# Optimization experiments

Hardware: AMD Instinct MI355X
Metric: run time of the kernel (lower is better)

## Reference

```python
import jax, jax.numpy as jnp
import numpy as np

B_SZ = 8
G = 2048
D_MODEL = 512
D_STATE = 128
D_CONV = 4
EXPAND = 2
HEADDIM = 64
D_INNER = EXPAND * D_MODEL          # 1024
NHEADS = D_INNER // HEADDIM         # 16
CONV_DIM = D_INNER + 2 * D_STATE    # 1280
D_IN_PROJ = 2 * D_INNER + 2 * D_STATE + NHEADS  # 2320
ID_DIM = 128
CHR_DIM = 64
N_CHR = 25
F_LOCUS = 32
PATH_DIM = 128
GENE_FEAT = ID_DIM + PATH_DIM + 2 * CHR_DIM  # 384
N_PERT = 10000
P_DIM = 128


def silu(x):
    return x * jax.nn.sigmoid(x)


def causal_dw_conv(x, w, b):
    # x: (B,L,C), w: (C,K), b: (C,)  causal depthwise conv (left pad K-1)
    K = w.shape[1]
    L = x.shape[1]
    xp = jnp.pad(x, ((0, 0), (K - 1, 0), (0, 0)))
    out = b[None, None, :]
    for k in range(K):
        out = out + xp[:, k:k + L, :] * w[:, k][None, None, :]
    return out


def mamba2(u, in_w, conv_w, conv_b, dt_bias, A_log, Dp, norm_w, out_w):
    # u: (B,L,d_model) -> (B,L,d_model); mamba_ssm Mamba2 defaults, ngroups=1
    Bb, L, _ = u.shape
    zxbcdt = u @ in_w.T                                   # (B,L,D_IN_PROJ)
    z = zxbcdt[..., :D_INNER]
    xBC = zxbcdt[..., D_INNER:D_INNER + CONV_DIM]
    dt = zxbcdt[..., D_INNER + CONV_DIM:]                 # (B,L,H)
    xBC = silu(causal_dw_conv(xBC, conv_w, conv_b))
    x = xBC[..., :D_INNER].reshape(Bb, L, NHEADS, HEADDIM)
    Bm = xBC[..., D_INNER:D_INNER + D_STATE]              # (B,L,N)
    Cm = xBC[..., D_INNER + D_STATE:]                     # (B,L,N)
    dt = jax.nn.softplus(dt + dt_bias)                    # (B,L,H)
    dA = jnp.exp(dt * (-jnp.exp(A_log)))                  # (B,L,H)

    def step(h, inp):
        dA_t, dt_t, B_t, C_t, x_t = inp
        h = dA_t[:, :, None, None] * h + jnp.einsum('bh,bn,bhp->bhpn', dt_t, B_t, x_t)
        y = jnp.einsum('bhpn,bn->bhp', h, C_t)
        return h, y

    h0 = jnp.zeros((Bb, NHEADS, HEADDIM, D_STATE), u.dtype)
    xs = (dA.transpose(1, 0, 2), dt.transpose(1, 0, 2),
          Bm.transpose(1, 0, 2), Cm.transpose(1, 0, 2), x.transpose(1, 0, 2, 3))
    _, ys = jax.lax.scan(step, h0, xs)                    # ys: (L,B,H,P)
    y = ys.transpose(1, 0, 2, 3) + Dp[None, None, :, None] * x
    y = y.reshape(Bb, L, D_INNER)
    # gated RMSNorm (norm_before_gate=False): norm(y * silu(z))
    y = y * silu(z)
    y = y * jax.lax.rsqrt(jnp.mean(y * y, axis=-1, keepdims=True) + 1e-5) * norm_w
    return y @ out_w.T


def setup_inputs() -> dict:
    key = jax.random.key(0)
    ks = iter(jax.random.split(key, 48))

    def nrm(shape, scale):
        return jax.random.normal(next(ks), shape, jnp.float32) * scale

    inp = {}
    inp['perturbation_idx'] = jax.random.randint(next(ks), (B_SZ,), 0, N_PERT)
    inp['chr_idx'] = jax.random.randint(next(ks), (G,), 0, N_CHR)
    inp['locus_fourier'] = nrm((G, 2 * F_LOCUS), 1.0)
    inp['pathway_features'] = nrm((G, PATH_DIM), 1.0)
    inp['pert_emb'] = nrm((N_PERT, P_DIM), 0.02)
    inp['gene_id_emb'] = nrm((G, ID_DIM), 0.02)
    inp['chr_emb'] = nrm((N_CHR, CHR_DIM), 0.02)
    inp['locus_w'] = nrm((CHR_DIM, 2 * F_LOCUS), (2 * F_LOCUS) ** -0.5)
    inp['locus_b'] = jnp.zeros((CHR_DIM,), jnp.float32)
    inp['cond_w'] = nrm((GENE_FEAT, P_DIM), P_DIM ** -0.5)
    inp['cond_b'] = jnp.zeros((GENE_FEAT,), jnp.float32)
    inp['in_w'] = nrm((D_MODEL, GENE_FEAT), GENE_FEAT ** -0.5)
    inp['in_b'] = jnp.zeros((D_MODEL,), jnp.float32)
    inp['head_w'] = nrm((1, D_MODEL), D_MODEL ** -0.5)
    inp['head_b'] = jnp.zeros((1,), jnp.float32)
    for p in ('f_', 'b_'):
        inp[p + 'in_w'] = nrm((D_IN_PROJ, D_MODEL), D_MODEL ** -0.5)
        inp[p + 'conv_w'] = nrm((CONV_DIM, D_CONV), D_CONV ** -0.5)
        inp[p + 'conv_b'] = jnp.zeros((CONV_DIM,), jnp.float32)
        inp[p + 'dt_bias'] = nrm((NHEADS,), 0.5)
        inp[p + 'A_log'] = jnp.log(jax.random.uniform(next(ks), (NHEADS,), jnp.float32, 1.0, 16.0))
        inp[p + 'D'] = jnp.ones((NHEADS,), jnp.float32)
        inp[p + 'norm_w'] = jnp.ones((D_INNER,), jnp.float32)
        inp[p + 'out_w'] = nrm((D_MODEL, D_INNER), D_INNER ** -0.5)
    return inp


def reference(perturbation_idx, chr_idx, locus_fourier, pathway_features,
              pert_emb, gene_id_emb, chr_emb, locus_w, locus_b,
              cond_w, cond_b, in_w, in_b, head_w, head_b,
              f_in_w, f_conv_w, f_conv_b, f_dt_bias, f_A_log, f_D, f_norm_w, f_out_w,
              b_in_w, b_conv_w, b_conv_b, b_dt_bias, b_A_log, b_D, b_norm_w, b_out_w):
    B = perturbation_idx.shape[0]
    cond = pert_emb[perturbation_idx] @ cond_w.T + cond_b          # (B, GENE_FEAT)
    e_chr = chr_emb[chr_idx]                                        # (G, CHR_DIM)
    e_locus = jax.nn.gelu(locus_fourier @ locus_w.T + locus_b, approximate=False)
    gene_feat = jnp.concatenate([gene_id_emb, pathway_features, e_chr, e_locus], axis=1)  # (G, GENE_FEAT)
    seq = jnp.concatenate([cond[:, None, :],
                           jnp.broadcast_to(gene_feat[None], (B,) + gene_feat.shape)], axis=1)
    seq = seq @ in_w.T + in_b                                       # (B, G+1, d_model)
    h_fwd = mamba2(seq, f_in_w, f_conv_w, f_conv_b, f_dt_bias, f_A_log, f_D, f_norm_w, f_out_w)
    h_bwd = jnp.flip(mamba2(jnp.flip(seq, axis=1), b_in_w, b_conv_w, b_conv_b,
                            b_dt_bias, b_A_log, b_D, b_norm_w, b_out_w), axis=1)
    H = h_fwd + h_bwd
    return H[:, 1:, :] @ head_w.T + head_b                          # (B, G, 1)
```

## Files before the change

kernel.cpp:

```cpp
#include <hip/hip_runtime.h>
#include <hip/hip_bf16.h>
#include <hip/hip_fp16.h>
#include <math.h>

#define DPROJ 2320
#define CONVD 1280

typedef __attribute__((ext_vector_type(8))) short bf16x8;
typedef __attribute__((ext_vector_type(4))) float f32x4;

__device__ __forceinline__ float siluf(float x) { return x / (1.f + __expf(-x)); }
__device__ __forceinline__ float bfu(unsigned short s) { return __uint_as_float(((unsigned)s) << 16); }
__device__ __forceinline__ unsigned short f2bf(float f) {
    unsigned u = __float_as_uint(f);
    unsigned r = (u + 0x7FFFu + ((u >> 16) & 1u)) >> 16;
    return (unsigned short)r;
}
__device__ __forceinline__ unsigned short f2h(float f) {
    __half h = __float2half(f);
    return *(unsigned short*)&h;
}
__device__ __forceinline__ float h2f(unsigned short s) {
    __half h = *(__half*)&s;
    return __half2float(h);
}


__global__ void gg_kernel(const int* __restrict__ chridx, const float* __restrict__ gid,
                          const float* __restrict__ path, const float* __restrict__ chrE,
                          const int* __restrict__ pidx, const float* __restrict__ pertE,
                          float* __restrict__ gf, float* __restrict__ cemb,
                          float* __restrict__ wf2, float* __restrict__ wb2) {
    int blk = blockIdx.x, tid = threadIdx.x;
    if (blk < 3072) {
        int idx = blk * 256 + tid;
        int g = idx / 384, j = idx % 384;
        float v;
        if (j < 128)      v = gid[(size_t)g * 128 + j];
        else if (j < 256) v = path[(size_t)g * 128 + (j - 128)];
        else if (j < 320) v = chrE[(size_t)chridx[g] * 64 + (j - 256)];
        else return;
        gf[idx] = v;
    } else if (blk < 3076) {
        int idx = (blk - 3072) * 256 + tid;
        int b = idx >> 7, k = idx & 127;
        cemb[idx] = pertE[(size_t)pidx[b] * 128 + k];
    } else {
        wf2[tid * 4 + 0] = 0.f; wf2[tid * 4 + 1] = 0.f;
        wf2[tid * 4 + 2] = 0.f; wf2[tid * 4 + 3] = 0.f;
        wb2[tid * 4 + 0] = 0.f; wb2[tid * 4 + 1] = 0.f;
        wb2[tid * 4 + 2] = 0.f; wb2[tid * 4 + 3] = 0.f;
    }
}

__global__ void wfold_kernel(const float* __restrict__ headW,
                             const float* __restrict__ fOutW, const float* __restrict__ fNw,
                             const float* __restrict__ bOutW, const float* __restrict__ bNw,
                             float* __restrict__ wf2, float* __restrict__ wb2) {
    int blk = blockIdx.x;
    int dir = blk >> 6;
    int rem = blk & 63;
    int dseg = rem >> 4, mseg = rem & 15;
    int tid = threadIdx.x;
    int d = dseg * 256 + tid;
    const float* W = dir ? bOutW : fOutW;
    float s = 0.f;
#pragma unroll
    for (int m = mseg * 32; m < mseg * 32 + 32; ++m)
        s += headW[m] * W[(size_t)m * 1024 + d];
    const float* nw = dir ? bNw : fNw;
    atomicAdd(&(dir ? wb2 : wf2)[d], s * nw[d]);
}


__global__ void tobf4_kernel(const float* __restrict__ inW, const float* __restrict__ fInW,
                             const float* __restrict__ bInW, const float* __restrict__ gf,
                             unsigned short* __restrict__ inW2, unsigned short* __restrict__ fInW2,
                             unsigned short* __restrict__ bInW2, unsigned short* __restrict__ gf2) {
    size_t idx = (size_t)blockIdx.x * 256 + threadIdx.x;
    const size_t A = 512UL * 384, B5 = 2432UL * 512;
    if (idx < A) {
        inW2[idx] = f2bf(inW[idx]);
    } else if (idx < A + B5) {
        size_t k = idx - A; int m = k / 512, kk = k % 512;
        fInW2[k] = f2bf(m < 2320 ? fInW[(size_t)m * 512 + kk] : 0.f);
    } else if (idx < A + 2 * B5) {
        size_t k = idx - A - B5; int m = k / 512, kk = k % 512;
        bInW2[k] = f2bf(m < 2320 ? bInW[(size_t)m * 512 + kk] : 0.f);
    } else {
        size_t k = idx - A - 2 * B5;
        gf2[k] = f2bf(gf[k]);
    }
}


__global__ __launch_bounds__(256) void mfma_gemm_kernel(
    const unsigned short* __restrict__ A2, const unsigned short* __restrict__ W2,
    const float* __restrict__ bias, float* __restrict__ C,
    unsigned short* __restrict__ Cbf, unsigned short* __restrict__ sz,
    int N, int K2, int ldc) {
    __shared__ __align__(16) unsigned short Al[128 * 40];
    __shared__ __align__(16) unsigned short Bl[128 * 40];
    const int tid = threadIdx.x;
    const int bm = blockIdx.y * 128, bn = blockIdx.x * 128;
    const int lane = tid & 63, wave = tid >> 6;
    const int wm = (wave >> 1) * 64, wn = (wave & 1) * 64;
    f32x4 acc[4][4];
#pragma unroll
    for (int i = 0; i < 4; ++i)
#pragma unroll
        for (int j = 0; j < 4; ++j) acc[i][j] = (f32x4){0.f, 0.f, 0.f, 0.f};

    for (int k0 = 0; k0 < K2; k0 += 32) {
        __syncthreads();
#pragma unroll
        for (int s = 0; s < 2; ++s) {
            int ch = tid + 256 * s;
            int row = ch >> 2, q = ch & 3;
            uint4 va = *(const uint4*)&A2[(size_t)(bm + row) * K2 + k0 + q * 8];
            *(uint4*)&Al[row * 40 + q * 8] = va;
            uint4 vb = *(const uint4*)&W2[(size_t)(bn + row) * K2 + k0 + q * 8];
            *(uint4*)&Bl[row * 40 + q * 8] = vb;
        }
        __syncthreads();
        bf16x8 af[4], bfr[4];
#pragma unroll
        for (int i = 0; i < 4; ++i)
            af[i] = *(const bf16x8*)&Al[(wm + i * 16 + (lane & 15)) * 40 + (lane >> 4) * 8];
#pragma unroll
        for (int j = 0; j < 4; ++j)
            bfr[j] = *(const bf16x8*)&Bl[(wn + j * 16 + (lane & 15)) * 40 + (lane >> 4) * 8];
#pragma unroll
        for (int i = 0; i < 4; ++i)
#pragma unroll
            for (int j = 0; j < 4; ++j)
                acc[i][j] = __builtin_amdgcn_mfma_f32_16x16x32_bf16(af[i], bfr[j], acc[i][j], 0, 0, 0);
    }
#pragma unroll
    for (int i = 0; i < 4; ++i) {
        int m = bm + wm + i * 16 + (lane >> 4) * 4;
#pragma unroll
        for (int j = 0; j < 4; ++j) {
            int n = bn + wn + j * 16 + (lane & 15);
            if (n < N) {
                float bv = bias ? bias[n] : 0.f;
#pragma unroll
                for (int r = 0; r < 4; ++r) {
                    float v = acc[i][j][r] + bv;
                    if (sz && n < 1024)
                        sz[(size_t)(m + r) * 1024 + n] = f2h(siluf(v));
                    else if (Cbf)
                        Cbf[(size_t)(m + r) * ldc + n] = f2bf(v);
                    else
                        C[(size_t)(m + r) * ldc + n] = v;
                }
            }
        }
    }
}


__global__ __launch_bounds__(256) void gemm_kernel(
    const float* __restrict__ A, const float* __restrict__ W,
    const float* __restrict__ bias, float* __restrict__ C,
    int M, int N, int K, int ldc, int act) {
    __shared__ __align__(16) float As[16][68];
    __shared__ __align__(16) float Ws[16][68];
    const int tid = threadIdx.x;
    const int tx = tid & 15, ty = tid >> 4;
    const int bm = blockIdx.y * 64, bn = blockIdx.x * 64;
    const int lr = tid >> 2;
    const int lk = (tid & 3) * 4;
    float acc[4][4];
#pragma unroll
    for (int i = 0; i < 4; ++i)
#pragma unroll
        for (int j = 0; j < 4; ++j) acc[i][j] = 0.f;

    for (int k0 = 0; k0 < K; k0 += 16) {
        const int am = bm + lr;
        const int wn = bn + lr;
        float4 av = make_float4(0.f, 0.f, 0.f, 0.f), wv = make_float4(0.f, 0.f, 0.f, 0.f);
        if (am < M) av = *(const float4*)&A[(size_t)am * K + k0 + lk];
        if (wn < N) wv = *(const float4*)&W[(size_t)wn * K + k0 + lk];
        __syncthreads();
        As[lk + 0][lr] = av.x; As[lk + 1][lr] = av.y; As[lk + 2][lr] = av.z; As[lk + 3][lr] = av.w;
        Ws[lk + 0][lr] = wv.x; Ws[lk + 1][lr] = wv.y; Ws[lk + 2][lr] = wv.z; Ws[lk + 3][lr] = wv.w;
        __syncthreads();
#pragma unroll
        for (int kk = 0; kk < 16; ++kk) {
            float4 a = *(const float4*)&As[kk][ty * 4];
            float4 w = *(const float4*)&Ws[kk][tx * 4];
            float aa[4] = {a.x, a.y, a.z, a.w}, ww[4] = {w.x, w.y, w.z, w.w};
#pragma unroll
            for (int i = 0; i < 4; ++i)
#pragma unroll
                for (int j = 0; j < 4; ++j) acc[i][j] += aa[i] * ww[j];
        }
    }
#pragma unroll
    for (int i = 0; i < 4; ++i) {
        const int m = bm + ty * 4 + i;
        if (m >= M) continue;
#pragma unroll
        for (int j = 0; j < 4; ++j) {
            const int n = bn + tx * 4 + j;
            if (n >= N) continue;
            float v = acc[i][j] + (bias ? bias[n] : 0.f);
            if (act == 1) v = 0.5f * v * (1.f + erff(v * 0.70710678118654752f));
            C[(size_t)m * ldc + n] = v;
        }
    }
}


__global__ void dt_kernel(const float* __restrict__ zxf, const float* __restrict__ zxb,
                          const float* __restrict__ zxc,
                          const float* __restrict__ fDtB, const float* __restrict__ bDtB,
                          float* __restrict__ dtFsT, float* __restrict__ dtBsT,
                          float* __restrict__ dtFp) {
    int idx = blockIdx.x * 256 + threadIdx.x;
    if (idx < 32768) {
        int r = idx >> 4, hh = idx & 15;
        float raw = zxf[(size_t)r * DPROJ + 2304 + hh] + fDtB[hh];
        dtFsT[hh * 2048 + r] = (raw > 20.f) ? raw : log1pf(expf(raw));
    } else if (idx < 65536) {
        int k = idx - 32768;
        int r = k >> 4, hh = k & 15;
        float raw = zxb[(size_t)(2047 - r) * DPROJ + 2304 + hh] + bDtB[hh];
        dtBsT[hh * 2048 + r] = (raw > 20.f) ? raw : log1pf(expf(raw));
    } else if (idx < 65664) {
        int k = idx - 65536;
        int b = k >> 4, hh = k & 15;
        float raw = zxc[(size_t)b * DPROJ + 2304 + hh] + fDtB[hh];
        dtFp[k] = (raw > 20.f) ? raw : log1pf(expf(raw));
    }
}

__global__ void cum_kernel(const float* __restrict__ dtFsT, const float* __restrict__ dtBsT,
                           const float* __restrict__ fAlog, const float* __restrict__ bAlog,
                           float* __restrict__ cumF, float* __restrict__ cumB) {
    int id = blockIdx.x * 256 + threadIdx.x;
    int dir = id >> 9, k = id & 511, h = k >> 5, c = k & 31;
    const float* dtT = dir ? dtBsT : dtFsT;
    const float* Al = dir ? bAlog : fAlog;
    float* cum = dir ? cumB : cumF;
    float a = -expf(Al[h]);
    float acc = 0.f;
    for (int s4 = 0; s4 < 16; ++s4) {
        float4 v = *(const float4*)&dtT[h * 2048 + c * 64 + s4 * 4];
        float4 o;
        acc += v.x * a; o.x = acc;
        acc += v.y * a; o.y = acc;
        acc += v.z * a; o.z = acc;
        acc += v.w * a; o.w = acc;
        *(float4*)&cum[h * 2048 + c * 64 + s4 * 4] = o;
    }
}


__global__ void convFsh_kernel(const float* __restrict__ zxf, const float* __restrict__ cw,
                               const float* __restrict__ cb,
                               unsigned short* __restrict__ bc16, unsigned short* __restrict__ x16) {
    int idx = blockIdx.x * 256 + threadIdx.x;
    if (idx >= 2045 * 1280) return;
    int t4 = idx / 1280, c = idx % 1280;
    float4 w4 = *(const float4*)&cw[c * 4];
    float acc = cb[c];
    acc += zxf[(size_t)(t4 + 0) * DPROJ + 1024 + c] * w4.x;
    acc += zxf[(size_t)(t4 + 1) * DPROJ + 1024 + c] * w4.y;
    acc += zxf[(size_t)(t4 + 2) * DPROJ + 1024 + c] * w4.z;
    acc += zxf[(size_t)(t4 + 3) * DPROJ + 1024 + c] * w4.w;
    float r = siluf(acc);
    if (c >= 1024) bc16[(size_t)t4 * 256 + (c - 1024)] = f2bf(r);
    else           x16[(size_t)t4 * 1024 + c] = f2bf(r);
}

__global__ void convFpb_kernel(const float* __restrict__ zxf, const float* __restrict__ zxc,
                               const float* __restrict__ cw, const float* __restrict__ cb,
                               float* __restrict__ outp, unsigned short* __restrict__ bc16,
                               unsigned short* __restrict__ x16) {
    int idx = blockIdx.x * 256 + threadIdx.x;
    int b = idx / 5120;
    int r = idx % 5120;
    int t = r / 1280, c = r % 1280;
    float4 w4 = *(const float4*)&cw[c * 4];
    float w[4] = {w4.x, w4.y, w4.z, w4.w};
    float acc = cb[c];
#pragma unroll
    for (int k = 0; k < 4; ++k) {
        int j = t - 3 + k;
        float x = 0.f;
        if (j == 0)      x = zxc[(size_t)b * DPROJ + 1024 + c];
        else if (j >= 1) x = zxf[(size_t)(j - 1) * DPROJ + 1024 + c];
        acc += x * w[k];
    }
    float rr = siluf(acc);
    outp[idx] = rr;
    if (c >= 1024) bc16[(size_t)(b * 4 + t) * 256 + (c - 1024)] = f2bf(rr);
    else           x16[(size_t)(b * 4 + t) * 1024 + c] = f2bf(rr);
}

__global__ void convBsh_kernel(const float* __restrict__ zxb, const float* __restrict__ cw,
                               const float* __restrict__ cb,
                               unsigned short* __restrict__ bc16, unsigned short* __restrict__ x16) {
    int idx = blockIdx.x * 256 + threadIdx.x;
    int s = idx / 1280, c = idx % 1280;
    float4 w4 = *(const float4*)&cw[c * 4];
    float w[4] = {w4.x, w4.y, w4.z, w4.w};
    float acc = cb[c];
#pragma unroll
    for (int k = 0; k < 4; ++k) {
        int j = s - 3 + k;
        if (j >= 0) acc += zxb[(size_t)(2047 - j) * DPROJ + 1024 + c] * w[k];
    }
    float r = siluf(acc);
    if (c >= 1024) bc16[(size_t)s * 256 + (c - 1024)] = f2bf(r);
    else           x16[(size_t)s * 1024 + c] = f2bf(r);
}


__global__ __launch_bounds__(256) void intra_kernel(
    const unsigned short* __restrict__ bcF, const unsigned short* __restrict__ bcFp,
    const unsigned short* __restrict__ bcB,
    const unsigned short* __restrict__ xF16, const unsigned short* __restrict__ xFp16,
    const unsigned short* __restrict__ xB16,
    const float* __restrict__ dtFsT, const float* __restrict__ dtBsT,
    const float* __restrict__ cumF, const float* __restrict__ cumB,
    unsigned short* __restrict__ YiF0, unsigned short* __restrict__ YiFs,
    unsigned short* __restrict__ YiB,
    unsigned short* __restrict__ UF0, unsigned short* __restrict__ UFs,
    unsigned short* __restrict__ UB) {
    __shared__ __align__(16) unsigned char smraw[63232];
    unsigned short* Bt = (unsigned short*)smraw;
    unsigned short* Ct = (unsigned short*)(smraw + 17408);
    unsigned short* Sm = (unsigned short*)(smraw + 17408);
    unsigned short* BT = (unsigned short*)(smraw + 34816);
    unsigned short* XT = (unsigned short*)(smraw + 53248);
    float* scum = (float*)(smraw + 62464);
    float* sdt  = scum + 64;
    float* se   = scum + 128;

    const int iid = blockIdx.x;
    int dir, b = 0, h, c;
    unsigned short *Yout, *Uout;
    if (iid < 128)      { dir = 0; b = iid >> 4; h = iid & 15; c = 0;
                          Yout = YiF0 + (size_t)(b * 16 + h) * 4096; Uout = UF0 + (size_t)(b * 16 + h) * 8192; }
    else if (iid < 624) { int k = iid - 128; dir = 0; c = 1 + (k >> 4); h = k & 15;
                          Yout = YiFs + (size_t)(c * 16 + h) * 4096; Uout = UFs + (size_t)(c * 16 + h) * 8192; }
    else                { int k = iid - 624; dir = 1; c = k >> 4; h = k & 15;
                          Yout = YiB + (size_t)(c * 16 + h) * 4096;  Uout = UB + (size_t)(c * 16 + h) * 8192; }
    const float* dtAT = dir ? dtBsT : dtFsT;
    const float* cumA = dir ? cumB : cumF;

    const int tid = threadIdx.x;
    const int lane = tid & 63, wave = tid >> 6;
    const int quad = lane >> 4, l15 = lane & 15;

    {
        int r = tid >> 2, q = tid & 3;
        const unsigned short *bsrc, *xsrc;
        if (dir == 0) {
            int t = 64 * c + 1 + r;
            if (t < 4) { bsrc = bcFp + (size_t)(b * 4 + t) * 256; xsrc = xFp16 + (size_t)(b * 4 + t) * 1024; }
            else       { bsrc = bcF + (size_t)(t - 4) * 256;      xsrc = xF16 + (size_t)(t - 4) * 1024; }
        } else {
            int s = 64 * c + r;
            bsrc = bcB + (size_t)s * 256;
            xsrc = xB16 + (size_t)s * 1024;
        }
#pragma unroll
        for (int i = 0; i < 4; ++i) {
            int n0 = q * 32 + i * 8;
            uint4 v = *(const uint4*)&bsrc[n0];
            *(uint4*)&Bt[r * 136 + n0] = v;
            const unsigned short* pv = (const unsigned short*)&v;
#pragma unroll
            for (int jj = 0; jj < 8; ++jj) BT[(n0 + jj) * 72 + r] = pv[jj];
        }
#pragma unroll
        for (int i = 0; i < 4; ++i) {
            int n0 = q * 32 + i * 8;
            uint4 v = *(const uint4*)&bsrc[128 + n0];
            *(uint4*)&Ct[r * 136 + n0] = v;
        }
#pragma unroll
        for (int k = 0; k < 2; ++k) {
            uint4 v = *(const uint4*)&xsrc[h * 64 + q * 16 + k * 8];
            const unsigned short* pv = (const unsigned short*)&v;
#pragma unroll
            for (int jj = 0; jj < 8; ++jj) XT[(q * 16 + k * 8 + jj) * 72 + r] = pv[jj];
        }
        if (tid < 64) {
            int j = 64 * c + tid;
            scum[tid] = cumA[h * 2048 + j];
            sdt[tid] = dtAT[h * 2048 + j];
        }
    }
    __syncthreads();
    if (tid < 64) se[tid] = __expf(scum[63] - scum[tid]) * sdt[tid];

    const int tm = (wave >> 1) * 32, sn = (wave & 1) * 32;
    f32x4 acc1[2][2];
#pragma unroll
    for (int i = 0; i < 2; ++i)
#pragma unroll
        for (int j = 0; j < 2; ++j) acc1[i][j] = (f32x4){0.f, 0.f, 0.f, 0.f};
#pragma unroll
    for (int ks = 0; ks < 4; ++ks) {
        bf16x8 af[2], bfr[2];
#pragma unroll
        for (int i = 0; i < 2; ++i)
            af[i] = *(const bf16x8*)&Ct[(tm + i * 16 + l15) * 136 + ks * 32 + quad * 8];
#pragma unroll
        for (int j = 0; j < 2; ++j)
            bfr[j] = *(const bf16x8*)&Bt[(sn + j * 16 + l15) * 136 + ks * 32 + quad * 8];
#pragma unroll
        for (int i = 0; i < 2; ++i)
#pragma unroll
            for (int j = 0; j < 2; ++j)
                acc1[i][j] = __builtin_amdgcn_mfma_f32_16x16x32_bf16(af[i], bfr[j], acc1[i][j], 0, 0, 0);
    }
    __syncthreads();

#pragma unroll
    for (int j = 0; j < 2; ++j) {
        int s = sn + j * 16 + l15;
        float cs = scum[s], ds = sdt[s];
#pragma unroll
        for (int i = 0; i < 2; ++i) {
#pragma unroll
            for (int r = 0; r < 4; ++r) {
                int t = tm + i * 16 + quad * 4 + r;
                float v = (s <= t) ? __expf(scum[t] - cs) * ds * acc1[i][j][r] : 0.f;
                Sm[t * 72 + s] = f2bf(v);
            }
        }
    }
    __syncthreads();

    const int pm = (wave >> 1) * 32, tn = (wave & 1) * 32;
    f32x4 acc2[2][2];
#pragma unroll
    for (int i = 0; i < 2; ++i)
#pragma unroll
        for (int j = 0; j < 2; ++j) acc2[i][j] = (f32x4){0.f, 0.f, 0.f, 0.f};
#pragma unroll
    for (int ks = 0; ks < 2; ++ks) {
        bf16x8 af[2], bfr[2];
#pragma unroll
        for (int i = 0; i < 2; ++i)
            af[i] = *(const bf16x8*)&XT[(pm + i * 16 + l15) * 72 + ks * 32 + quad * 8];
#pragma unroll
        for (int j = 0; j < 2; ++j)
            bfr[j] = *(const bf16x8*)&Sm[(tn + j * 16 + l15) * 72 + ks * 32 + quad * 8];
#pragma unroll
        for (int i = 0; i < 2; ++i)
#pragma unroll
            for (int j = 0; j < 2; ++j)
                acc2[i][j] = __builtin_amdgcn_mfma_f32_16x16x32_bf16(af[i], bfr[j], acc2[i][j], 0, 0, 0);
    }
#pragma unroll
    for (int i = 0; i < 2; ++i)
#pragma unroll
        for (int j = 0; j < 2; ++j) {
            int t = tn + j * 16 + l15;
            int p0 = pm + i * 16 + quad * 4;
            ushort4 o = make_ushort4(f2bf(acc2[i][j][0]), f2bf(acc2[i][j][1]),
                                     f2bf(acc2[i][j][2]), f2bf(acc2[i][j][3]));
            *(ushort4*)&Yout[t * 64 + p0] = o;
        }

    const int nm = wave * 32;
    f32x4 acc3[2][4];
#pragma unroll
    for (int i = 0; i < 2; ++i)
#pragma unroll
        for (int j = 0; j < 4; ++j) acc3[i][j] = (f32x4){0.f, 0.f, 0.f, 0.f};
#pragma unroll
    for (int ks = 0; ks < 2; ++ks) {
        float ev[8];
#pragma unroll
        for (int jj = 0; jj < 8; ++jj) ev[jj] = se[ks * 32 + quad * 8 + jj];
        bf16x8 bfx[4];
#pragma unroll
        for (int j = 0; j < 4; ++j) {
            bf16x8 xs = *(const bf16x8*)&XT[(j * 16 + l15) * 72 + ks * 32 + quad * 8];
#pragma unroll
            for (int jj = 0; jj < 8; ++jj)
                bfx[j][jj] = (short)f2bf(bfu((unsigned short)xs[jj]) * ev[jj]);
        }
        bf16x8 af[2];
#pragma unroll
        for (int i = 0; i < 2; ++i)
            af[i] = *(const bf16x8*)&BT[(nm + i * 16 + l15) * 72 + ks * 32 + quad * 8];
#pragma unroll
        for (int i = 0; i < 2; ++i)
#pragma unroll
            for (int j = 0; j < 4; ++j)
                acc3[i][j] = __builtin_amdgcn_mfma_f32_16x16x32_bf16(af[i], bfx[j], acc3[i][j], 0, 0, 0);
    }
#pragma unroll
    for (int i = 0; i < 2; ++i)
#pragma unroll
        for (int j = 0; j < 4; ++j) {
            int p = j * 16 + l15;
            int n0 = nm + i * 16 + quad * 4;
            ushort4 o = make_ushort4(f2bf(acc3[i][j][0]), f2bf(acc3[i][j][1]),
                                     f2bf(acc3[i][j][2]), f2bf(acc3[i][j][3]));
            *(ushort4*)&Uout[p * 128 + n0] = o;
        }
}


__global__ void cbm_kernel(const float* __restrict__ convFp, const unsigned short* __restrict__ bcF,
                           const float* __restrict__ dtFp, const float* __restrict__ cumF,
                           const unsigned short* __restrict__ UF0,
                           float* __restrict__ cb0, unsigned short* __restrict__ Mb) {
    int blk = blockIdx.x, tid = threadIdx.x;
    if (blk < 32) {
        int idx = blk * 256 + tid;
        int b = idx >> 10, r = idx & 1023, h = r >> 6, tl = r & 63;
        int t = tl + 1;
        const float* b0 = convFp + (size_t)(b * 4) * CONVD;
        float s = 0.f;
        if (t < 4) {
            const float* crow = convFp + (size_t)(b * 4 + t) * CONVD;
            for (int n = 0; n < 128; ++n) s += crow[1152 + n] * b0[1024 + n];
        } else {
            const unsigned short* cr = bcF + (size_t)(t - 4) * 256 + 128;
            for (int n = 0; n < 128; ++n) s += bfu(cr[n]) * b0[1024 + n];
        }
        cb0[(b * 16 + h) * 64 + tl] = s * dtFp[b * 16 + h];
    } else {
        int bh = blk - 32;
        int b = bh >> 4, h = bh & 15;
        float D0 = __expf(cumF[h * 2048 + 63]);
        float dt0 = dtFp[b * 16 + h];
        const float* row0 = convFp + (size_t)(b * 4) * CONVD;
        const unsigned short* u = UF0 + (size_t)(b * 16 + h) * 8192;
        unsigned short* m = Mb + (size_t)(b * 16 + h) * 8192;
        for (int e4 = tid; e4 < 2048; e4 += 256) {
            int e = e4 * 4, p = e >> 7, n0 = e & 127;
            float s = D0 * dt0 * row0[h * 64 + p];
            float4 B4 = *(const float4*)&row0[1024 + n0];
            ushort4 uv = *(const ushort4*)&u[e];
            ushort4 o = make_ushort4(f2bf(s * B4.x + bfu(uv.x)), f2bf(s * B4.y + bfu(uv.y)),
                                     f2bf(s * B4.z + bfu(uv.z)), f2bf(s * B4.w + bfu(uv.w)));
            *(ushort4*)&m[e] = o;
        }
    }
}


__global__ void tpsi_kernel(const unsigned short* __restrict__ UFs, const unsigned short* __restrict__ UB,
                            const float* __restrict__ cumF, const float* __restrict__ cumB,
                            unsigned short* __restrict__ Tst, float* __restrict__ psiF) {
    int blk = blockIdx.x;
    int dir = blk >> 7, h = (blk >> 3) & 15, q8 = blk & 7;
    int tid = threadIdx.x;
    const unsigned short* U = dir ? UB : UFs;
    const float* cum = dir ? cumB : cumF;
    unsigned short* T = Tst + (size_t)(dir * 16 + h) * 32 * 8192;
    if (dir == 0 && q8 == 0 && tid == 0) {
        float ps = 1.f;
        for (int c = 1; c < 32; ++c) {
            psiF[h * 32 + c] = ps;
            ps *= __expf(cumF[h * 2048 + c * 64 + 63]);
        }
    }
    const size_t e = (size_t)q8 * 1024 + 4 * tid;
    float4 st = make_float4(0.f, 0.f, 0.f, 0.f);
    const int c0 = dir ? 0 : 1;
    ushort4 u = *(const ushort4*)&U[((size_t)c0 * 16 + h) * 8192 + e];
    for (int c = c0; c < 32; ++c) {
        ushort4 un = make_ushort4(0, 0, 0, 0);
        if (c + 1 < 32) un = *(const ushort4*)&U[((size_t)(c + 1) * 16 + h) * 8192 + e];
        float Dc = __expf(cum[h * 2048 + c * 64 + 63]);
        ushort4 o = make_ushort4(f2bf(st.x), f2bf(st.y), f2bf(st.z), f2bf(st.w));
        *(ushort4*)&T[(size_t)c * 8192 + e] = o;
        st.x = Dc * st.x + bfu(u.x);
        st.y = Dc * st.y + bfu(u.y);
        st.z = Dc * st.z + bfu(u.z);
        st.w = Dc * st.w + bfu(u.w);
        u = un;
    }
}


__global__ __launch_bounds__(256) void yt_kernel(
    const unsigned short* __restrict__ bcF, const unsigned short* __restrict__ bcB,
    const unsigned short* __restrict__ Tst,
    unsigned short* __restrict__ YtF, unsigned short* __restrict__ YtB) {
    const int iid = blockIdx.x;
    int dir, h, c;
    if (iid < 496) { dir = 0; c = 1 + (iid >> 4); h = iid & 15; }
    else           { int k = iid - 496; dir = 1; c = k >> 4; h = k & 15; }
    const unsigned short* Cbase = (dir == 0)
        ? bcF + ((size_t)(64 * c - 3)) * 256 + 128
        : bcB + ((size_t)(64 * c)) * 256 + 128;
    const unsigned short* Tp = Tst + ((size_t)(dir * 16 + h) * 32 + c) * 8192;
    unsigned short* Yt = (dir == 0 ? YtF : YtB) + (size_t)(c * 16 + h) * 4096;
    const int tid = threadIdx.x;
    const int lane = tid & 63, wave = tid >> 6;
    const int quad = lane >> 4, l15 = lane & 15;
    const int pm = (wave >> 1) * 32, tb = (wave & 1) * 32;
    f32x4 acc[2][2];
#pragma unroll
    for (int i = 0; i < 2; ++i)
#pragma unroll
        for (int j = 0; j < 2; ++j) acc[i][j] = (f32x4){0.f, 0.f, 0.f, 0.f};
#pragma unroll
    for (int ks = 0; ks < 4; ++ks) {
        bf16x8 af[2], bfr[2];
#pragma unroll
        for (int i = 0; i < 2; ++i)
            af[i] = *(const bf16x8*)&Tp[(size_t)(pm + i * 16 + l15) * 128 + ks * 32 + quad * 8];
#pragma unroll
        for (int j = 0; j < 2; ++j)
            bfr[j] = *(const bf16x8*)&Cbase[(size_t)(tb + j * 16 + l15) * 256 + ks * 32 + quad * 8];
#pragma unroll
        for (int i = 0; i < 2; ++i)
#pragma unroll
            for (int j = 0; j < 2; ++j)
                acc[i][j] = __builtin_amdgcn_mfma_f32_16x16x32_bf16(af[i], bfr[j], acc[i][j], 0, 0, 0);
    }
#pragma unroll
    for (int i = 0; i < 2; ++i)
#pragma unroll
        for (int j = 0; j < 2; ++j) {
            int t = tb + j * 16 + l15;
            int p0 = pm + i * 16 + quad * 4;
            ushort4 o = make_ushort4(f2bf(acc[i][j][0]), f2bf(acc[i][j][1]),
                                     f2bf(acc[i][j][2]), f2bf(acc[i][j][3]));
            *(ushort4*)&Yt[t * 64 + p0] = o;
        }
}


__global__ __launch_bounds__(256) void gate_kernel(
    const unsigned short* __restrict__ bcF,
    const unsigned short* __restrict__ Mb, const float* __restrict__ psiF,
    const unsigned short* __restrict__ YtF, const unsigned short* __restrict__ YtB,
    const unsigned short* __restrict__ xF16, const unsigned short* __restrict__ xFp16,
    const unsigned short* __restrict__ xB16,
    const unsigned short* __restrict__ szF, const unsigned short* __restrict__ szB,
    const float* __restrict__ convFp,
    const float* __restrict__ cumF, const float* __restrict__ cumB,
    const unsigned short* __restrict__ YiF0, const unsigned short* __restrict__ YiFs,
    const unsigned short* __restrict__ YiB,
    const float* __restrict__ cb0,
    const float* __restrict__ fD, const float* __restrict__ bD,
    const float* __restrict__ wf2, const float* __restrict__ wb2,
    float* __restrict__ aF, float* __restrict__ aB) {
    __shared__ __align__(16) float Ysm[64 * 68];

    const int iid = blockIdx.x;
    int dir, b = 0, h, cg;
    if (iid < 1024) { dir = 0; b = iid >> 7; int r = iid & 127; h = r >> 3; cg = r & 7; }
    else            { int k = iid - 1024; dir = 1; h = k >> 3; cg = k & 7; }
    const int tid = threadIdx.x, tx = tid & 15, ty = tid >> 4;
    const int lane = tid & 63, wave = tid >> 6;
    const int quad = lane >> 4, l15 = lane & 15;

    const float Dh = (dir ? bD : fD)[h];
    const float* wvp = dir ? wb2 : wf2;
    float4 wreg = *(const float4*)&wvp[h * 64 + tx * 4];
    const float* cumA = dir ? cumB : cumF;

    const int pm = (wave >> 1) * 32, tb = (wave & 1) * 32;
    bf16x8 mfr[4][2];
    if (dir == 0) {
        const unsigned short* Mp = Mb + (size_t)(b * 16 + h) * 8192;
#pragma unroll
        for (int ks = 0; ks < 4; ++ks)
#pragma unroll
            for (int i = 0; i < 2; ++i)
                mfr[ks][i] = *(const bf16x8*)&Mp[(size_t)(pm + i * 16 + l15) * 128 + ks * 32 + quad * 8];
    }

    for (int cc = 0; cc < 4; ++cc) {
        const int c = cg * 4 + cc;
        const bool fwdG = (dir == 0 && c > 0);
        if (fwdG) {
            if (cc > 0) __syncthreads();
            const unsigned short* Cbase = bcF + ((size_t)(64 * c - 3)) * 256 + 128;
            f32x4 acc[2][2];
#pragma unroll
            for (int i = 0; i < 2; ++i)
#pragma unroll
                for (int j = 0; j < 2; ++j) acc[i][j] = (f32x4){0.f, 0.f, 0.f, 0.f};
#pragma unroll
            for (int ks = 0; ks < 4; ++ks) {
                bf16x8 bfr[2];
#pragma unroll
                for (int j = 0; j < 2; ++j)
                    bfr[j] = *(const bf16x8*)&Cbase[(size_t)(tb + j * 16 + l15) * 256 + ks * 32 + quad * 8];
#pragma unroll
                for (int i = 0; i < 2; ++i)
#pragma unroll
                    for (int j = 0; j < 2; ++j)
                        acc[i][j] = __builtin_amdgcn_mfma_f32_16x16x32_bf16(mfr[ks][i], bfr[j], acc[i][j], 0, 0, 0);
            }
#pragma unroll
            for (int i = 0; i < 2; ++i)
#pragma unroll
                for (int j = 0; j < 2; ++j)
                    *(f32x4*)&Ysm[(tb + j * 16 + l15) * 68 + pm + i * 16 + quad * 4] = acc[i][j];
            __syncthreads();
        }

        const float psi = fwdG ? psiF[h * 32 + c] : 0.f;
        const unsigned short* Ytp = fwdG ? (YtF + (size_t)(c * 16 + h) * 4096)
                                         : (dir ? (YtB + (size_t)(c * 16 + h) * 4096) : nullptr);
        float4 x0v = make_float4(0.f, 0.f, 0.f, 0.f);
        float cbv[4] = {0.f, 0.f, 0.f, 0.f};
        if (dir == 0 && c == 0) {
            x0v = *(const float4*)&convFp[(size_t)(b * 4) * CONVD + h * 64 + tx * 4];
#pragma unroll
            for (int i = 0; i < 4; ++i) cbv[i] = cb0[(b * 16 + h) * 64 + (ty + 16 * i)];
        }

        float rawet[4];
        ushort4 yi4a[4], x4a[4], z4a[4], yt4a[4];
        float4 cm4a[4];
#pragma unroll
        for (int i = 0; i < 4; ++i) {
            int tl = ty + 16 * i;
            int j = 64 * c + tl;
            rawet[i] = cumA[h * 2048 + j];
            const unsigned short *Yi, *xp, *zp;
            if (dir == 0) {
                Yi = (c == 0) ? YiF0 + (size_t)(b * 16 + h) * 4096 : YiFs + (size_t)(c * 16 + h) * 4096;
                if (c == 0) {
                    int t = j + 1;
                    xp = (t < 4) ? xFp16 + (size_t)(b * 4 + t) * 1024 : xF16 + (size_t)(t - 4) * 1024;
                } else {
                    xp = xF16 + (size_t)(64 * c + tl - 3) * 1024;
                }
                zp = szF + (size_t)j * 1024;
            } else {
                Yi = YiB + (size_t)(c * 16 + h) * 4096;
                xp = xB16 + (size_t)j * 1024;
                zp = szB + (size_t)(2047 - j) * 1024;
            }
            yi4a[i] = *(const ushort4*)&Yi[tl * 64 + tx * 4];
            x4a[i] = *(const ushort4*)&xp[h * 64 + tx * 4];
            z4a[i] = *(const ushort4*)&zp[h * 64 + tx * 4];
            yt4a[i] = Ytp ? *(const ushort4*)&Ytp[tl * 64 + tx * 4] : make_ushort4(0, 0, 0, 0);
            cm4a[i] = fwdG ? *(const float4*)&Ysm[tl * 68 + tx * 4] : make_float4(0.f, 0.f, 0.f, 0.f);
        }

#pragma unroll
        for (int i = 0; i < 4; ++i) {
            int j = 64 * c + ty + 16 * i;
            float et = __expf(rawet[i]);
            float yv[4] = {bfu(yi4a[i].x), bfu(yi4a[i].y), bfu(yi4a[i].z), bfu(yi4a[i].w)};
            float xa[4] = {bfu(x4a[i].x), bfu(x4a[i].y), bfu(x4a[i].z), bfu(x4a[i].w)};
            float sza[4] = {h2f(z4a[i].x), h2f(z4a[i].y), h2f(z4a[i].z), h2f(z4a[i].w)};
            float ya[4] = {bfu(yt4a[i].x) + psi * cm4a[i].x, bfu(yt4a[i].y) + psi * cm4a[i].y,
                           bfu(yt4a[i].z) + psi * cm4a[i].z, bfu(yt4a[i].w) + psi * cm4a[i].w};
            float x0a[4] = {x0v.x, x0v.y, x0v.z, x0v.w};
            float wa[4] = {wreg.x, wreg.y, wreg.z, wreg.w};
            float a1 = 0.f, a2 = 0.f;
#pragma unroll
            for (int w = 0; w < 4; ++w) {
                float tot = yv[w] + et * (ya[w] + cbv[i] * x0a[w]) + Dh * xa[w];
                float g = tot * sza[w];
                a1 += g * wa[w];
                a2 += g * g;
            }
#pragma unroll
            for (int m = 1; m < 16; m <<= 1) {
                a1 += __shfl_xor(a1, m);
                a2 += __shfl_xor(a2, m);
            }
            if (tx == 0) {
                if (dir == 0) {
                    size_t o = ((size_t)(b * 2048 + j) * 16 + h) * 2;
                    aF[o] = a1; aF[o + 1] = a2;
                } else {
                    int g = 2047 - j;
                    size_t o = ((size_t)g * 16 + h) * 2;
                    aB[o] = a1; aB[o + 1] = a2;
                }
            }
        }
    }
}


__global__ void final_kernel(const float* __restrict__ aF, const float* __restrict__ aB,
                             const float* __restrict__ headB, float* __restrict__ out) {
    int idx = blockIdx.x * 256 + threadIdx.x;
    int b = idx >> 11, g = idx & 2047;
    const float* pf = aF + ((size_t)(b * 2048 + g)) * 32;
    const float* pb = aB + (size_t)g * 32;
    float f1 = 0.f, f2 = 0.f, b1 = 0.f, b2 = 0.f;
#pragma unroll
    for (int h = 0; h < 16; ++h) {
        f1 += pf[2 * h]; f2 += pf[2 * h + 1];
        b1 += pb[2 * h]; b2 += pb[2 * h + 1];
    }
    out[idx] = f1 * rsqrtf(f2 * (1.f / 1024.f) + 1e-5f) +
               b1 * rsqrtf(b2 * (1.f / 1024.f) + 1e-5f) + headB[0];
}


extern "C" void kernel_launch(void* const* d_in, const int* in_sizes, int n_in,
                              void* d_out, int out_size, void* d_ws, size_t ws_size,
                              hipStream_t stream) {
    const int*   pidx   = (const int*)  d_in[0];
    const int*   chridx = (const int*)  d_in[1];
    const float* locusF = (const float*)d_in[2];
    const float* pathF  = (const float*)d_in[3];
    const float* pertE  = (const float*)d_in[4];
    const float* gidE   = (const float*)d_in[5];
    const float* chrE   = (const float*)d_in[6];
    const float* locusW = (const float*)d_in[7];
    const float* locusB = (const float*)d_in[8];
    const float* condW  = (const float*)d_in[9];
    const float* condB  = (const float*)d_in[10];
    const float* inW    = (const float*)d_in[11];
    const float* inB    = (const float*)d_in[12];
    const float* headW  = (const float*)d_in[13];
    const float* headB  = (const float*)d_in[14];
    const float* fInW   = (const float*)d_in[15];
    const float* fCw    = (const float*)d_in[16];
    const float* fCb    = (const float*)d_in[17];
    const float* fDtB   = (const float*)d_in[18];
    const float* fAlog  = (const float*)d_in[19];
    const float* fDp    = (const float*)d_in[20];
    const float* fNw    = (const float*)d_in[21];
    const float* fOutW  = (const float*)d_in[22];
    const float* bInW   = (const float*)d_in[23];
    const float* bCw    = (const float*)d_in[24];
    const float* bCb    = (const float*)d_in[25];
    const float* bDtB   = (const float*)d_in[26];
    const float* bAlog  = (const float*)d_in[27];
    const float* bDp    = (const float*)d_in[28];
    const float* bNw    = (const float*)d_in[29];
    const float* bOutW  = (const float*)d_in[30];
    float* out = (float*)d_out;
    (void)in_sizes; (void)n_in; (void)out_size; (void)ws_size;

    char* base = (char*)d_ws;
    size_t off = 0;
    auto allocf = [&](size_t n) -> float* {
        char* r = base + off; off += ((n * 4 + 63) & ~(size_t)63); return (float*)r; };
    auto allocu = [&](size_t n) -> unsigned short* {
        char* r = base + off; off += ((n * 2 + 63) & ~(size_t)63); return (unsigned short*)r; };

    float* gf     = allocf(2048UL * 384);
    float* cond   = allocf(8UL * 384);
    float* cemb   = allocf(8UL * 128);
    float* uc     = allocf(8UL * 512);
    float* zxf    = allocf(2048UL * DPROJ);
    float* zxb    = allocf(2048UL * DPROJ);
    float* zxc    = allocf(8UL * DPROJ);
    float* convFp = allocf(8UL * 4 * CONVD);
    float* dtFsT  = allocf(16UL * 2048);
    float* dtFp   = allocf(128);
    float* dtBsT  = allocf(16UL * 2048);
    float* cumF   = allocf(16UL * 2048);
    float* cumB   = allocf(16UL * 2048);
    float* wf2    = allocf(1024);
    float* wb2    = allocf(1024);
    float* cb0    = allocf(8UL * 16 * 64);
    float* psiF   = allocf(16UL * 32);
    float* aF     = allocf(8UL * 2048 * 16 * 2);
    float* aB     = allocf(2048UL * 16 * 2);
    unsigned short* YiF0 = allocu(8UL * 16 * 4096);
    unsigned short* YiFs = allocu(32UL * 16 * 4096);
    unsigned short* YiB  = allocu(32UL * 16 * 4096);
    unsigned short* UF0  = allocu(8UL * 16 * 8192);
    unsigned short* UFs  = allocu(32UL * 16 * 8192);
    unsigned short* UB   = allocu(32UL * 16 * 8192);
    unsigned short* Mb   = allocu(8UL * 16 * 8192);
    unsigned short* Tst  = allocu(2UL * 16 * 32 * 8192);
    unsigned short* bcF  = allocu(2045UL * 256);
    unsigned short* bcFp = allocu(32UL * 256);
    unsigned short* bcB  = allocu(2048UL * 256);
    unsigned short* YtF  = allocu(32UL * 16 * 4096);
    unsigned short* YtB  = allocu(32UL * 16 * 4096);
    unsigned short* xF16 = allocu(2045UL * 1024);
    unsigned short* xFp16= allocu(32UL * 1024);
    unsigned short* xB16 = allocu(2048UL * 1024);
    unsigned short* szF  = allocu(2048UL * 1024);
    unsigned short* szB  = allocu(2048UL * 1024);
    unsigned short* gf2   = allocu(2048UL * 384);
    unsigned short* inW2  = allocu(512UL * 384);
    unsigned short* ug2   = allocu(2048UL * 512);
    unsigned short* fInW2 = allocu(2432UL * 512);
    unsigned short* bInW2 = allocu(2432UL * 512);

    gg_kernel<<<3077, 256, 0, stream>>>(chridx, gidE, pathF, chrE, pidx, pertE, gf, cemb, wf2, wb2);
    wfold_kernel<<<128, 256, 0, stream>>>(headW, fOutW, fNw, bOutW, bNw, wf2, wb2);
    gemm_kernel<<<dim3(1, 32), 256, 0, stream>>>(locusF, locusW, locusB, gf + 320, 2048, 64, 64, 384, 1);
    gemm_kernel<<<dim3(6, 1), 256, 0, stream>>>(cemb, condW, condB, cond, 8, 384, 128, 384, 0);

    tobf4_kernel<<<13568, 256, 0, stream>>>(inW, fInW, bInW, gf, inW2, fInW2, bInW2, gf2);

    mfma_gemm_kernel<<<dim3(4, 16), 256, 0, stream>>>(gf2, inW2, inB, nullptr, ug2, nullptr, 512, 384, 512);
    gemm_kernel<<<dim3(8, 1), 256, 0, stream>>>(cond, inW, inB, uc, 8, 512, 384, 512, 0);

    mfma_gemm_kernel<<<dim3(19, 16), 256, 0, stream>>>(ug2, fInW2, nullptr, zxf, nullptr, szF, 2320, 512, DPROJ);
    mfma_gemm_kernel<<<dim3(19, 16), 256, 0, stream>>>(ug2, bInW2, nullptr, zxb, nullptr, szB, 2320, 512, DPROJ);
    gemm_kernel<<<dim3(37, 1), 256, 0, stream>>>(uc, fInW, nullptr, zxc, 8, DPROJ, 512, DPROJ, 0);

    dt_kernel<<<257, 256, 0, stream>>>(zxf, zxb, zxc, fDtB, bDtB, dtFsT, dtBsT, dtFp);
    cum_kernel<<<4, 256, 0, stream>>>(dtFsT, dtBsT, fAlog, bAlog, cumF, cumB);
    convFsh_kernel<<<(2045 * 1280 + 255) / 256, 256, 0, stream>>>(zxf, fCw, fCb, bcF, xF16);
    convFpb_kernel<<<160, 256, 0, stream>>>(zxf, zxc, fCw, fCb, convFp, bcFp, xFp16);
    convBsh_kernel<<<10240, 256, 0, stream>>>(zxb, bCw, bCb, bcB, xB16);
    intra_kernel<<<1136, 256, 0, stream>>>(bcF, bcFp, bcB, xF16, xFp16, xB16,
                                           dtFsT, dtBsT, cumF, cumB,
                                           YiF0, YiFs, YiB, UF0, UFs, UB);
    cbm_kernel<<<160, 256, 0, stream>>>(convFp, bcF, dtFp, cumF, UF0, cb0, Mb);
    tpsi_kernel<<<256, 256, 0, stream>>>(UFs, UB, cumF, cumB, Tst, psiF);
    yt_kernel<<<1008, 256, 0, stream>>>(bcF, bcB, Tst, YtF, YtB);
    gate_kernel<<<1152, 256, 0, stream>>>(bcF, Mb, psiF, YtF, YtB, xF16, xFp16, xB16,
                                          szF, szB, convFp, cumF, cumB,
                                          YiF0, YiFs, YiB, cb0, fDp, bDp, wf2, wb2, aF, aB);
    final_kernel<<<64, 256, 0, stream>>>(aF, aB, headB, out);
}
```

Before: 397.2 us.

## Store in-proj xBC outputs as bf16 in compact buffers and merge conv kernels

The in-projection GEMM epilogue now writes the xBC slice as compact bf16 rows of 1280 and the dt slice as a small fp32 buffer, replacing the full fp32 2320-wide zxf/zxb outputs. The three depthwise conv kernels are merged into one launch that reads the bf16 buffers. This halves the intermediate write and read traffic and removes two kernel launches. The cost is an extra bf16 rounding of the pre-conv activations.

```diff
diff --git a/kernel.cpp b/kernel.cpp
--- a/kernel.cpp
+++ b/kernel.cpp
@@ -96,8 +96,9 @@
 
 __global__ __launch_bounds__(256) void mfma_gemm_kernel(
     const unsigned short* __restrict__ A2, const unsigned short* __restrict__ W2,
-    const float* __restrict__ bias, float* __restrict__ C,
+    const float* __restrict__ bias,
     unsigned short* __restrict__ Cbf, unsigned short* __restrict__ sz,
+    unsigned short* __restrict__ xbc, float* __restrict__ dtr,
     int N, int K2, int ldc) {
     __shared__ __align__(16) unsigned short Al[128 * 40];
     __shared__ __align__(16) unsigned short Bl[128 * 40];
@@ -147,12 +148,15 @@
 #pragma unroll
                 for (int r = 0; r < 4; ++r) {
                     float v = acc[i][j][r] + bv;
-                    if (sz && n < 1024)
+                    if (Cbf) {
+                        Cbf[(size_t)(m + r) * ldc + n] = f2bf(v);
+                    } else if (n < 1024) {
                         sz[(size_t)(m + r) * 1024 + n] = f2h(siluf(v));
-                    else if (Cbf)
-                        Cbf[(size_t)(m + r) * ldc + n] = f2bf(v);
-                    else
-                        C[(size_t)(m + r) * ldc + n] = v;
+                    } else if (n < 2304) {
+                        xbc[(size_t)(m + r) * 1280 + (n - 1024)] = f2bf(v);
+                    } else {
+                        dtr[(size_t)(m + r) * 16 + (n - 2304)] = v;
+                    }
                 }
             }
         }
@@ -214,7 +218,7 @@
 }
 
 
-__global__ void dt_kernel(const float* __restrict__ zxf, const float* __restrict__ zxb,
+__global__ void dt_kernel(const float* __restrict__ dtrF, const float* __restrict__ dtrB,
                           const float* __restrict__ zxc,
                           const float* __restrict__ fDtB, const float* __restrict__ bDtB,
                           float* __restrict__ dtFsT, float* __restrict__ dtBsT,
@@ -222,12 +226,12 @@
     int idx = blockIdx.x * 256 + threadIdx.x;
     if (idx < 32768) {
         int r = idx >> 4, hh = idx & 15;
-        float raw = zxf[(size_t)r * DPROJ + 2304 + hh] + fDtB[hh];
+        float raw = dtrF[idx] + fDtB[hh];
         dtFsT[hh * 2048 + r] = (raw > 20.f) ? raw : log1pf(expf(raw));
     } else if (idx < 65536) {
         int k = idx - 32768;
         int r = k >> 4, hh = k & 15;
-        float raw = zxb[(size_t)(2047 - r) * DPROJ + 2304 + hh] + bDtB[hh];
+        float raw = dtrB[(size_t)(2047 - r) * 16 + hh] + bDtB[hh];
         dtBsT[hh * 2048 + r] = (raw > 20.f) ? raw : log1pf(expf(raw));
     } else if (idx < 65664) {
         int k = idx - 65536;
@@ -259,64 +263,64 @@
 }
 
 
-__global__ void convFsh_kernel(const float* __restrict__ zxf, const float* __restrict__ cw,
-                               const float* __restrict__ cb,
-                               unsigned short* __restrict__ bc16, unsigned short* __restrict__ x16) {
-    int idx = blockIdx.x * 256 + threadIdx.x;
-    if (idx >= 2045 * 1280) return;
-    int t4 = idx / 1280, c = idx % 1280;
-    float4 w4 = *(const float4*)&cw[c * 4];
-    float acc = cb[c];
-    acc += zxf[(size_t)(t4 + 0) * DPROJ + 1024 + c] * w4.x;
-    acc += zxf[(size_t)(t4 + 1) * DPROJ + 1024 + c] * w4.y;
-    acc += zxf[(size_t)(t4 + 2) * DPROJ + 1024 + c] * w4.z;
-    acc += zxf[(size_t)(t4 + 3) * DPROJ + 1024 + c] * w4.w;
-    float r = siluf(acc);
-    if (c >= 1024) bc16[(size_t)t4 * 256 + (c - 1024)] = f2bf(r);
-    else           x16[(size_t)t4 * 1024 + c] = f2bf(r);
-}
-
-__global__ void convFpb_kernel(const float* __restrict__ zxf, const float* __restrict__ zxc,
-                               const float* __restrict__ cw, const float* __restrict__ cb,
-                               float* __restrict__ outp, unsigned short* __restrict__ bc16,
-                               unsigned short* __restrict__ x16) {
-    int idx = blockIdx.x * 256 + threadIdx.x;
-    int b = idx / 5120;
-    int r = idx % 5120;
-    int t = r / 1280, c = r % 1280;
-    float4 w4 = *(const float4*)&cw[c * 4];
-    float w[4] = {w4.x, w4.y, w4.z, w4.w};
-    float acc = cb[c];
-#pragma unroll
-    for (int k = 0; k < 4; ++k) {
-        int j = t - 3 + k;
-        float x = 0.f;
-        if (j == 0)      x = zxc[(size_t)b * DPROJ + 1024 + c];
-        else if (j >= 1) x = zxf[(size_t)(j - 1) * DPROJ + 1024 + c];
-        acc += x * w[k];
-    }
-    float rr = siluf(acc);
-    outp[idx] = rr;
-    if (c >= 1024) bc16[(size_t)(b * 4 + t) * 256 + (c - 1024)] = f2bf(rr);
-    else           x16[(size_t)(b * 4 + t) * 1024 + c] = f2bf(rr);
-}
-
-__global__ void convBsh_kernel(const float* __restrict__ zxb, const float* __restrict__ cw,
-                               const float* __restrict__ cb,
-                               unsigned short* __restrict__ bc16, unsigned short* __restrict__ x16) {
-    int idx = blockIdx.x * 256 + threadIdx.x;
-    int s = idx / 1280, c = idx % 1280;
-    float4 w4 = *(const float4*)&cw[c * 4];
-    float w[4] = {w4.x, w4.y, w4.z, w4.w};
-    float acc = cb[c];
-#pragma unroll
-    for (int k = 0; k < 4; ++k) {
-        int j = s - 3 + k;
-        if (j >= 0) acc += zxb[(size_t)(2047 - j) * DPROJ + 1024 + c] * w[k];
-    }
-    float r = siluf(acc);
-    if (c >= 1024) bc16[(size_t)s * 256 + (c - 1024)] = f2bf(r);
-    else           x16[(size_t)s * 1024 + c] = f2bf(r);
+__global__ void conv_kernel(const unsigned short* __restrict__ xbcF,
+                            const unsigned short* __restrict__ xbcB,
+                            const float* __restrict__ zxc,
+                            const float* __restrict__ fCw, const float* __restrict__ fCb,
+                            const float* __restrict__ bCw, const float* __restrict__ bCb,
+                            unsigned short* __restrict__ bcF, unsigned short* __restrict__ xF16,
+                            unsigned short* __restrict__ bcB, unsigned short* __restrict__ xB16,
+                            float* __restrict__ convFp, unsigned short* __restrict__ bcFp,
+                            unsigned short* __restrict__ xFp16) {
+    int blk = blockIdx.x, tid = threadIdx.x;
+    if (blk < 10225) {
+        int idx = blk * 256 + tid;
+        if (idx >= 2045 * 1280) return;
+        int t4 = idx / 1280, c = idx % 1280;
+        float4 w4 = *(const float4*)&fCw[c * 4];
+        float acc = fCb[c];
+        acc += bfu(xbcF[(size_t)(t4 + 0) * 1280 + c]) * w4.x;
+        acc += bfu(xbcF[(size_t)(t4 + 1) * 1280 + c]) * w4.y;
+        acc += bfu(xbcF[(size_t)(t4 + 2) * 1280 + c]) * w4.z;
+        acc += bfu(xbcF[(size_t)(t4 + 3) * 1280 + c]) * w4.w;
+        float r = siluf(acc);
+        if (c >= 1024) bcF[(size_t)t4 * 256 + (c - 1024)] = f2bf(r);
+        else           xF16[(size_t)t4 * 1024 + c] = f2bf(r);
+    } else if (blk < 20465) {
+        int idx = (blk - 10225) * 256 + tid;
+        int s = idx / 1280, c = idx % 1280;
+        float4 w4 = *(const float4*)&bCw[c * 4];
+        float w[4] = {w4.x, w4.y, w4.z, w4.w};
+        float acc = bCb[c];
+#pragma unroll
+        for (int k = 0; k < 4; ++k) {
+            int j = s - 3 + k;
+            if (j >= 0) acc += bfu(xbcB[(size_t)(2047 - j) * 1280 + c]) * w[k];
+        }
+        float r = siluf(acc);
+        if (c >= 1024) bcB[(size_t)s * 256 + (c - 1024)] = f2bf(r);
+        else           xB16[(size_t)s * 1024 + c] = f2bf(r);
+    } else {
+        int idx = (blk - 20465) * 256 + tid;
+        int b = idx / 5120;
+        int r = idx % 5120;
+        int t = r / 1280, c = r % 1280;
+        float4 w4 = *(const float4*)&fCw[c * 4];
+        float w[4] = {w4.x, w4.y, w4.z, w4.w};
+        float acc = fCb[c];
+#pragma unroll
+        for (int k = 0; k < 4; ++k) {
+            int j = t - 3 + k;
+            float x = 0.f;
+            if (j == 0)      x = zxc[(size_t)b * DPROJ + 1024 + c];
+            else if (j >= 1) x = bfu(xbcF[(size_t)(j - 1) * 1280 + c]);
+            acc += x * w[k];
+        }
+        float rr = siluf(acc);
+        convFp[idx] = rr;
+        if (c >= 1024) bcFp[(size_t)(b * 4 + t) * 256 + (c - 1024)] = f2bf(rr);
+        else           xFp16[(size_t)(b * 4 + t) * 1024 + c] = f2bf(rr);
+    }
 }
 
 
@@ -855,10 +859,10 @@
     float* cond   = allocf(8UL * 384);
     float* cemb   = allocf(8UL * 128);
     float* uc     = allocf(8UL * 512);
-    float* zxf    = allocf(2048UL * DPROJ);
-    float* zxb    = allocf(2048UL * DPROJ);
     float* zxc    = allocf(8UL * DPROJ);
     float* convFp = allocf(8UL * 4 * CONVD);
+    float* dtrF   = allocf(2048UL * 16);
+    float* dtrB   = allocf(2048UL * 16);
     float* dtFsT  = allocf(16UL * 2048);
     float* dtFp   = allocf(128);
     float* dtBsT  = allocf(16UL * 2048);
@@ -870,6 +874,8 @@
     float* psiF   = allocf(16UL * 32);
     float* aF     = allocf(8UL * 2048 * 16 * 2);
     float* aB     = allocf(2048UL * 16 * 2);
+    unsigned short* xbcF = allocu(2048UL * 1280);
+    unsigned short* xbcB = allocu(2048UL * 1280);
     unsigned short* YiF0 = allocu(8UL * 16 * 4096);
     unsigned short* YiFs = allocu(32UL * 16 * 4096);
     unsigned short* YiB  = allocu(32UL * 16 * 4096);
@@ -901,18 +907,17 @@
 
     tobf4_kernel<<<13568, 256, 0, stream>>>(inW, fInW, bInW, gf, inW2, fInW2, bInW2, gf2);
 
-    mfma_gemm_kernel<<<dim3(4, 16), 256, 0, stream>>>(gf2, inW2, inB, nullptr, ug2, nullptr, 512, 384, 512);
+    mfma_gemm_kernel<<<dim3(4, 16), 256, 0, stream>>>(gf2, inW2, inB, ug2, nullptr, nullptr, nullptr, 512, 384, 512);
     gemm_kernel<<<dim3(8, 1), 256, 0, stream>>>(cond, inW, inB, uc, 8, 512, 384, 512, 0);
 
-    mfma_gemm_kernel<<<dim3(19, 16), 256, 0, stream>>>(ug2, fInW2, nullptr, zxf, nullptr, szF, 2320, 512, DPROJ);
-    mfma_gemm_kernel<<<dim3(19, 16), 256, 0, stream>>>(ug2, bInW2, nullptr, zxb, nullptr, szB, 2320, 512, DPROJ);
+    mfma_gemm_kernel<<<dim3(19, 16), 256, 0, stream>>>(ug2, fInW2, nullptr, nullptr, szF, xbcF, dtrF, 2320, 512, 0);
+    mfma_gemm_kernel<<<dim3(19, 16), 256, 0, stream>>>(ug2, bInW2, nullptr, nullptr, szB, xbcB, dtrB, 2320, 512, 0);
     gemm_kernel<<<dim3(37, 1), 256, 0, stream>>>(uc, fInW, nullptr, zxc, 8, DPROJ, 512, DPROJ, 0);
 
-    dt_kernel<<<257, 256, 0, stream>>>(zxf, zxb, zxc, fDtB, bDtB, dtFsT, dtBsT, dtFp);
+    dt_kernel<<<257, 256, 0, stream>>>(dtrF, dtrB, zxc, fDtB, bDtB, dtFsT, dtBsT, dtFp);
     cum_kernel<<<4, 256, 0, stream>>>(dtFsT, dtBsT, fAlog, bAlog, cumF, cumB);
-    convFsh_kernel<<<(2045 * 1280 + 255) / 256, 256, 0, stream>>>(zxf, fCw, fCb, bcF, xF16);
-    convFpb_kernel<<<160, 256, 0, stream>>>(zxf, zxc, fCw, fCb, convFp, bcFp, xFp16);
-    convBsh_kernel<<<10240, 256, 0, stream>>>(zxb, bCw, bCb, bcB, xB16);
+    conv_kernel<<<20625, 256, 0, stream>>>(xbcF, xbcB, zxc, fCw, fCb, bCw, bCb,
+                                           bcF, xF16, bcB, xB16, convFp, bcFp, xFp16);
     intra_kernel<<<1136, 256, 0, stream>>>(bcF, bcFp, bcB, xF16, xFp16, xB16,
                                            dtFsT, dtBsT, cumF, cumB,
                                            YiF0, YiFs, YiB, UF0, UFs, UB);
```

Result: faster. 389.2 us (-2.0%).
